# Kernel optimization log

Measured on AMD Instinct MI355X. Metric: run time of the kernel, lower is better.

Reference implementation:

```python
import jax, jax.numpy as jnp
import numpy as np

# static config (mirrors params)
T, B, NA, NF = 48, 256, 23, 4
D = NA * NF          # y_dim = 92
XD = 2               # x_dim
H = 128              # rnn_dim
HD = 128             # h_dim
NL = 2               # n_layers
FS = 0.1
BURN = 12
IN_ENC = XD + D + H  # GRU input size = 222
A0, A1 = 12, 11      # agents 0..11 -> net0, 12..22 -> net1


def setup_inputs() -> dict:
    key = jax.random.key(0)
    ks = jax.random.split(key, 16)
    s = 0.05
    rn = lambda k, shape: jax.random.normal(k, shape, jnp.float32) * s
    return {
        "states": jax.random.normal(ks[0], (T + 1, 1, B, D), jnp.float32),
        # per-network (leading dim 2) GRU layer-0 and layer-1 weights (torch GRU layout: [r|z|n])
        "W_ih0": rn(ks[1], (2, 3 * H, IN_ENC)),
        "W_hh0": rn(ks[2], (2, 3 * H, H)),
        "b_ih0": rn(ks[3], (2, 3 * H)),
        "b_hh0": rn(ks[4], (2, 3 * H)),
        "W_ih1": rn(ks[5], (2, 3 * H, H)),
        "W_hh1": rn(ks[6], (2, 3 * H, H)),
        "b_ih1": rn(ks[7], (2, 3 * H)),
        "b_hh1": rn(ks[8], (2, 3 * H)),
        # decoder MLP (dropout is identity in eval) + mean head
        "W1": rn(ks[9], (2, HD, H)),
        "b1": rn(ks[10], (2, HD)),
        "W2": rn(ks[11], (2, HD, HD)),
        "b2": rn(ks[12], (2, HD)),
        "Wm": rn(ks[13], (2, XD, HD)),
        "bm": rn(ks[14], (2, XD)),
        "rollout": 0,
        "train": 0,
    }


def _gru_cell(x, h, Wih, Whh, bih, bhh):
    gi = x @ Wih.T + bih
    gh = h @ Whh.T + bhh
    r = jax.nn.sigmoid(gi[:, :H] + gh[:, :H])
    z = jax.nn.sigmoid(gi[:, H:2 * H] + gh[:, H:2 * H])
    n = jnp.tanh(gi[:, 2 * H:] + r * gh[:, 2 * H:])
    return (1.0 - z) * n + z * h


def _batch_error(a, b):
    # sum over batch of the euclidean norm over features
    return jnp.sum(jnp.sqrt(jnp.sum((a - b) ** 2, axis=1)))


def _group_step(h, y_t, y3, y3n, lo, hi, g, P):
    # h: [NL, A*B, H]; agents lo..hi-1 of network g, folded into the batch dim
    A = hi - lo
    vel = y3[:, lo:hi, 2:4].transpose(1, 0, 2).reshape(A * B, 2)
    pos = y3[:, lo:hi, 0:2].transpose(1, 0, 2).reshape(A * B, 2)
    vel_true = y3n[:, lo:hi, 2:4].transpose(1, 0, 2).reshape(A * B, 2)
    pos_true = y3n[:, lo:hi, 0:2].transpose(1, 0, 2).reshape(A * B, 2)
    y_rep = jnp.broadcast_to(y_t[None], (A, B, D)).reshape(A * B, D)
    h_last = h[-1]
    enc_in = jnp.concatenate([vel, y_rep, h_last], axis=1)  # [A*B, IN_ENC]
    # decoder uses the PRE-update hidden state
    d = jax.nn.relu(h_last @ P["W1"][g].T + P["b1"][g])
    d = jax.nn.relu(d @ P["W2"][g].T + P["b2"][g])
    dm = d @ P["Wm"][g].T + P["bm"][g]  # [A*B, XD]
    # 2-layer GRU step
    h0n = _gru_cell(enc_in, h[0], P["W_ih0"][g], P["W_hh0"][g], P["b_ih0"][g], P["b_hh0"][g])
    h1n = _gru_cell(h0n, h[1], P["W_ih1"][g], P["W_hh1"][g], P["b_ih1"][g], P["b_hh1"][g])
    h_new = jnp.stack([h0n, h1n])
    L = _batch_error(dm, vel_true)
    ep = _batch_error(pos + vel * FS, pos_true)
    ev = _batch_error(dm[:, :2], vel_true)
    return h_new, L, ep, ev


def _forward(states, P):
    y_seq = states[:T, 0]       # [T, B, D]
    y_next = states[1:T + 1, 0]  # [T, B, D]

    def step(carry, xs):
        h0, h1, L, ep, ev = carry
        y_t, y_t1, t = xs
        y3 = y_t.reshape(B, NA, NF)
        y3n = y_t1.reshape(B, NA, NF)
        h0n, L0, ep0, ev0 = _group_step(h0, y_t, y3, y3n, 0, A0, 0, P)
        h1n, L1, ep1, ev1 = _group_step(h1, y_t, y3, y3n, A0, NA, 1, P)
        m = (t >= BURN).astype(jnp.float32)
        return (h0n, h1n, L + L0 + L1, ep + m * (ep0 + ep1), ev + m * (ev0 + ev1)), None

    init = (jnp.zeros((NL, A0 * B, H), jnp.float32),
            jnp.zeros((NL, A1 * B, H), jnp.float32),
            jnp.zeros((), jnp.float32), jnp.zeros((), jnp.float32), jnp.zeros((), jnp.float32))
    (h0, h1, L, ep, ev), _ = jax.lax.scan(step, init, (y_seq, y_next, jnp.arange(T)))
    L_rec = L / (T * NA)
    e_pos = ep / ((T - BURN) * NA)
    e_vel = ev / ((T - BURN) * NA)
    return L_rec, e_pos, e_vel


def reference(states, W_ih0, W_hh0, b_ih0, b_hh0, W_ih1, W_hh1, b_ih1, b_hh1,
              W1, b1, W2, b2, Wm, bm, rollout, train):
    P = dict(W_ih0=W_ih0, W_hh0=W_hh0, b_ih0=b_ih0, b_hh0=b_hh0,
             W_ih1=W_ih1, W_hh1=W_hh1, b_ih1=b_ih1, b_hh1=b_hh1,
             W1=W1, b1=b1, W2=W2, b2=b2, Wm=Wm, bm=bm)
    return _forward(states, P)
```

## Files before the change

kernel.cpp:

```cpp
#include <hip/hip_runtime.h>
#include <hip/hip_bf16.h>


typedef unsigned short u16;
typedef unsigned int u32;
typedef unsigned char u8;
typedef __attribute__((ext_vector_type(4))) float f32x4;
typedef __attribute__((ext_vector_type(8))) int i32x8;

#define MFMA128(acc, a, b) \
  (acc) = __builtin_amdgcn_mfma_scale_f32_16x16x128_f8f6f4( \
      (a), (b), (acc), 0, 0, 0, 0x7F7F7F7F, 0, 0x7F7F7F7F)

__device__ __forceinline__ i32x8 ld8(const u8* p) { return *(const i32x8*)p; }
__device__ __forceinline__ void pinV(i32x8& x) { asm volatile("" : "+v"(x)); }

__device__ __forceinline__ u8 f2e4(float v) {
  return (u8)(__builtin_amdgcn_cvt_pk_fp8_f32(v, 0.f, 0, false) & 0xff);
}
__device__ __forceinline__ u32 pk4(float a, float b, float c, float d) {
  u32 p = (u32)__builtin_amdgcn_cvt_pk_fp8_f32(a, b, 0, false);
  return (u32)__builtin_amdgcn_cvt_pk_fp8_f32(c, d, (int)p, true);
}
__device__ __forceinline__ float sigf(float x) {
  return __builtin_amdgcn_rcpf(1.f + __expf(-x));
}
__device__ __forceinline__ float tanh_fast(float x) {
  return 1.f - 2.f * __builtin_amdgcn_rcpf(1.f + __expf(2.f * x));
}

constexpr int E0 = 2 * 384 * 352;
constexpr int E1 = E0 + 2 * 384 * 256;
constexpr int E2 = E1 + 2 * 128 * 128;
constexpr int E3 = E2 + 2 * 128 * 128;
constexpr int E4 = E3 + 2 * 128 * 128;
constexpr int E5 = E4 + 2 * 128 * 128;
constexpr int NBIAS = 2048;
constexpr int TOTAL = E5 + NBIAS + 4;
constexpr int WB_BYTE_OFF = 16384;

constexpr int WB0A_REL = E5;
constexpr int YBG2_REL = WB0A_REL + 23 * 384 * 128;
constexpr int NA1 = TOTAL;
constexpr int NA2 = NA1 + 23 * 384 * 128;
constexpr int NA3 = NA2 + 48 * 256 * 128;

__global__ void prep_kernel(const float* __restrict__ states,
                            const float* __restrict__ Wih0, const float* __restrict__ Whh0,
                            const float* __restrict__ bih0, const float* __restrict__ bhh0,
                            const float* __restrict__ Wih1, const float* __restrict__ Whh1,
                            const float* __restrict__ bih1, const float* __restrict__ bhh1,
                            const float* __restrict__ W1, const float* __restrict__ W2,
                            u8* __restrict__ wb, float* __restrict__ wsf) {
  for (int idx = blockIdx.x * blockDim.x + threadIdx.x; idx < NA3;
       idx += gridDim.x * blockDim.x) {
    if (idx < E0) {
      int g = idx / 135168;
      int r = idx - g * 135168;
      int j = r / 352;
      int k = r - j * 352;
      const float* wi = Wih0 + (g * 384 + j) * 222;
      float v;
      if (k < 94) v = wi[k];
      else if (k < 96) v = 0.f;
      else if (k < 224) v = wi[k - 2];
      else v = Whh0[(g * 384 + j) * 128 + (k - 224)];
      wb[idx] = f2e4(v);
    } else if (idx < E1) {
      int q = idx - E0;
      int g = q / 98304;
      int r = q - g * 98304;
      int j = r >> 8;
      int k = r & 255;
      float v = (k < 128) ? Wih1[(g * 384 + j) * 128 + k]
                          : Whh1[(g * 384 + j) * 128 + (k - 128)];
      wb[idx] = f2e4(v);
    } else if (idx < E2) {
      wb[idx] = 0;
    } else if (idx < E3) {
      int q = idx - E2; int g = q >> 14; int r = q & 16383; int j = r >> 7; int k = r & 127;
      wb[idx] = f2e4(W1[(g * 128 + j) * 128 + k]);
    } else if (idx < E4) {
      int q = idx - E3; int g = q >> 14; int r = q & 16383; int j = r >> 7; int k = r & 127;
      wb[idx] = f2e4(W2[(g * 128 + j) * 128 + k]);
    } else if (idx < E5) {
      wb[idx] = 0;
    } else if (idx < E5 + NBIAS) {
      int q = idx - E5;
      float v;
      if (q < 512)       { int g = q >> 8, j = q & 255;              v = bih0[g*384 + j] + bhh0[g*384 + j]; }
      else if (q < 768)  { int p = q - 512;  int g = p >> 7, j = p & 127; v = bih0[g*384 + 256 + j]; }
      else if (q < 1024) { int p = q - 768;  int g = p >> 7, j = p & 127; v = bhh0[g*384 + 256 + j]; }
      else if (q < 1536) { int p = q - 1024; int g = p >> 8, j = p & 255; v = bih1[g*384 + j] + bhh1[g*384 + j]; }
      else if (q < 1792) { int p = q - 1536; int g = p >> 7, j = p & 127; v = bih1[g*384 + 256 + j]; }
      else               { int p = q - 1792; int g = p >> 7, j = p & 127; v = bhh1[g*384 + 256 + j]; }
      wsf[4 + q] = v;
    } else if (idx < TOTAL) {
      wsf[idx - (E5 + NBIAS)] = 0.f;
    } else if (idx < NA2) {
      int q = idx - NA1;
      int a = q / 49152;
      int r = q - a * 49152;
      int j = r >> 7;
      int k = r & 127;
      const float* wi = Wih0 + (((a >= 12) ? 1 : 0) * 384 + j) * 222;
      float v = (k < 92) ? wi[2 + k] : 0.f;
      if (k == a * 4 + 2) v += wi[0];
      if (k == a * 4 + 3) v += wi[1];
      wb[WB0A_REL + q] = f2e4(v);
    } else {
      int q = idx - NA2;
      int t = q >> 15;
      int r = q & 32767;
      int row = r >> 7;
      int k = r & 127;
      float v = (k < 92) ? states[((size_t)t * 256 + row) * 92 + k] : 0.f;
      wb[YBG2_REL + q] = f2e4(v);
    }
  }
}

__global__ __launch_bounds__(512, 2) __attribute__((amdgpu_waves_per_eu(2, 2)))
void rnn_kernel(const float* __restrict__ states,
                const u8* __restrict__ wb,
                float* __restrict__ wsf,
                const float* __restrict__ b1g,
                const float* __restrict__ b2g,
                const float* __restrict__ Wmg,
                const float* __restrict__ bmg) {
  const int blk = blockIdx.x;
  const int g = (blk < 96) ? 0 : 1;
  const int r0 = (g == 0) ? (blk * 32) : ((blk - 96) * 32);
  const int aAg = (g == 0 ? 0 : 12) + (r0 >> 8);
  const int b0 = r0 & 255;

  const int tid = threadIdx.x;
  const int wid = tid >> 6;
  const int ln = tid & 63;
  const int j_in = ln & 15;
  const int kq = ln >> 4;
  const int c0 = wid * 16 + kq * 4;
  const int jh = wid * 16 + j_in;

  __shared__ __align__(16) u8 h0b[2][32 * 144];
  __shared__ __align__(16) u8 h1b[2][32 * 144];
  __shared__ __align__(16) u8 d1b[32 * 144];
  __shared__ __align__(16) u8 d2b[32 * 144];
  __shared__ __align__(16) float bias[1536];
  __shared__ float dmv[48][32][2];
  __shared__ float red[8][3];

  const u8* W0   = wb + g * 135168;
  const u8* W1c  = wb + E0 + g * 98304;
  const u8* Wm1p = wb + E2 + g * 16384;
  const u8* Wm2p = wb + E3 + g * 16384;
  const u8* WB0A = wb + WB0A_REL + aAg * 49152;
  const u8* YBG  = wb + YBG2_REL;

  i32x8 w0r0 = ld8(WB0A + jh * 128 + kq * 32);
  i32x8 w0r1 = ld8(W0 + jh * 352 + 96 + kq * 32);
  i32x8 w0r2 = ld8(W0 + jh * 352 + 224 + kq * 32);
  i32x8 w0z0 = ld8(WB0A + (128 + jh) * 128 + kq * 32);
  i32x8 w0z1 = ld8(W0 + (128 + jh) * 352 + 96 + kq * 32);
  i32x8 w0z2 = ld8(W0 + (128 + jh) * 352 + 224 + kq * 32);
  i32x8 w0n0 = ld8(WB0A + (256 + jh) * 128 + kq * 32);
  i32x8 w0n1 = ld8(W0 + (256 + jh) * 352 + 96 + kq * 32);
  i32x8 wn0  = ld8(W0 + (256 + jh) * 352 + 224 + kq * 32);
  i32x8 w1r0 = ld8(W1c + jh * 256 + kq * 32);
  i32x8 w1r1 = ld8(W1c + jh * 256 + 128 + kq * 32);
  i32x8 w1z0 = ld8(W1c + (128 + jh) * 256 + kq * 32);
  i32x8 w1z1 = ld8(W1c + (128 + jh) * 256 + 128 + kq * 32);
  i32x8 w1n0 = ld8(W1c + (256 + jh) * 256 + kq * 32);
  i32x8 wn1  = ld8(W1c + (256 + jh) * 256 + 128 + kq * 32);
  i32x8 wm1  = ld8(Wm1p + jh * 128 + kq * 32);
  i32x8 wm2  = ld8(Wm2p + jh * 128 + kq * 32);
  pinV(w0r0); pinV(w0r1); pinV(w0r2);
  pinV(w0z0); pinV(w0z1); pinV(w0z2);
  pinV(w0n0); pinV(w0n1); pinV(wn0);
  pinV(w1r0); pinV(w1r1); pinV(w1z0); pinV(w1z1);
  pinV(w1n0); pinV(wn1); pinV(wm1); pinV(wm2);

  for (int i = tid; i < 1536; i += 512) {
    float v;
    if (i < 256)       v = wsf[4 + g * 256 + i];
    else if (i < 384)  v = wsf[516 + g * 128 + (i - 256)];
    else if (i < 512)  v = wsf[772 + g * 128 + (i - 384)];
    else if (i < 768)  v = wsf[1028 + g * 256 + (i - 512)];
    else if (i < 896)  v = wsf[1540 + g * 128 + (i - 768)];
    else if (i < 1024) v = wsf[1796 + g * 128 + (i - 896)];
    else if (i < 1152) v = b1g[g * 128 + (i - 1024)];
    else if (i < 1280) v = b2g[g * 128 + (i - 1152)];
    else               v = Wmg[g * 256 + (i - 1280)];
    bias[i] = v;
  }
  for (int i = tid; i < 32 * 144; i += 512) { h0b[0][i] = 0; h1b[0][i] = 0; }

  f32x4 hv0[2] = {{0,0,0,0},{0,0,0,0}};
  f32x4 hv1[2] = {{0,0,0,0},{0,0,0,0}};
  __syncthreads();

  for (int t = 0; t < 48; ++t) {
    const int cur = t & 1, nxt = cur ^ 1;
    const u8* h0c = h0b[cur]; u8* h0n = h0b[nxt];
    const u8* h1c = h1b[cur]; u8* h1n = h1b[nxt];
    const u8* yt = YBG + t * 32768;

    {
      f32x4 b1v = *(const f32x4*)(bias + 1024 + c0);
      f32x4 brv = *(const f32x4*)(bias + c0);
      f32x4 bzv = *(const f32x4*)(bias + 128 + c0);
      f32x4 biv = *(const f32x4*)(bias + 256 + c0);
      f32x4 bhv = *(const f32x4*)(bias + 384 + c0);
#pragma unroll
      for (int nt = 0; nt < 2; ++nt) {
        const int row = nt * 16 + j_in;
        i32x8 fy  = ld8(yt + (b0 + row) * 128 + kq * 32);
        i32x8 fh1 = ld8(h1c + row * 144 + kq * 32);
        i32x8 fh0 = ld8(h0c + row * 144 + kq * 32);
        f32x4 mm = {0,0,0,0};
        MFMA128(mm, wm1, fh1);
        f32x4 aR = {0,0,0,0}, aZ = {0,0,0,0}, aN = {0,0,0,0}, aG = {0,0,0,0};
        MFMA128(aR, w0r0, fy);  MFMA128(aZ, w0z0, fy);  MFMA128(aN, w0n0, fy);
        MFMA128(aR, w0r1, fh1); MFMA128(aZ, w0z1, fh1); MFMA128(aN, w0n1, fh1);
        MFMA128(aR, w0r2, fh0); MFMA128(aZ, w0z2, fh0); MFMA128(aG, wn0, fh0);
        *(u32*)(d1b + row * 144 + c0) =
          pk4(fmaxf(mm[0]+b1v[0],0.f), fmaxf(mm[1]+b1v[1],0.f),
              fmaxf(mm[2]+b1v[2],0.f), fmaxf(mm[3]+b1v[3],0.f));
#pragma unroll
        for (int i = 0; i < 4; ++i) {
          float rv = sigf(aR[i] + brv[i]);
          float zv = sigf(aZ[i] + bzv[i]);
          float nv = tanh_fast(aN[i] + biv[i] + rv * (aG[i] + bhv[i]));
          hv0[nt][i] = (1.f - zv) * nv + zv * hv0[nt][i];
        }
      }
    }
    __syncthreads();

#pragma unroll
    for (int nt = 0; nt < 2; ++nt)
      *(u32*)(h0n + (nt * 16 + j_in) * 144 + c0) = pk4(hv0[nt][0], hv0[nt][1], hv0[nt][2], hv0[nt][3]);
    {
      f32x4 b2v = *(const f32x4*)(bias + 1152 + c0);
#pragma unroll
      for (int nt = 0; nt < 2; ++nt) {
        const int row = nt * 16 + j_in;
        i32x8 fd1 = ld8(d1b + row * 144 + kq * 32);
        f32x4 mm = {0,0,0,0};
        MFMA128(mm, wm2, fd1);
        *(u32*)(d2b + row * 144 + c0) =
          pk4(fmaxf(mm[0]+b2v[0],0.f), fmaxf(mm[1]+b2v[1],0.f),
              fmaxf(mm[2]+b2v[2],0.f), fmaxf(mm[3]+b2v[3],0.f));
      }
    }
    __syncthreads();

    {
      f32x4 brv = *(const f32x4*)(bias + 512 + c0);
      f32x4 bzv = *(const f32x4*)(bias + 640 + c0);
      f32x4 biv = *(const f32x4*)(bias + 768 + c0);
      f32x4 bhv = *(const f32x4*)(bias + 896 + c0);
#pragma unroll
      for (int nt = 0; nt < 2; ++nt) {
        const int row = nt * 16 + j_in;
        i32x8 fg0 = ld8(h0n + row * 144 + kq * 32);
        i32x8 fh1 = ld8(h1c + row * 144 + kq * 32);
        f32x4 aR = {0,0,0,0}, aZ = {0,0,0,0}, aN = {0,0,0,0}, aG = {0,0,0,0};
        MFMA128(aR, w1r0, fg0); MFMA128(aZ, w1z0, fg0); MFMA128(aN, w1n0, fg0);
        MFMA128(aR, w1r1, fh1); MFMA128(aZ, w1z1, fh1); MFMA128(aG, wn1, fh1);
#pragma unroll
        for (int i = 0; i < 4; ++i) {
          float rv = sigf(aR[i] + brv[i]);
          float zv = sigf(aZ[i] + bzv[i]);
          float nv = tanh_fast(aN[i] + biv[i] + rv * (aG[i] + bhv[i]));
          hv1[nt][i] = (1.f - zv) * nv + zv * hv1[nt][i];
        }
        *(u32*)(h1n + row * 144 + c0) = pk4(hv1[nt][0], hv1[nt][1], hv1[nt][2], hv1[nt][3]);
      }
      {
        int row = tid >> 4, c = (tid >> 3) & 1, part = tid & 7;
        const u8* dp = d2b + row * 144 + part * 16;
        const float* wmr = bias + 1280 + c * 128 + part * 16;
        float s = 0.f;
#pragma unroll
        for (int q = 0; q < 4; ++q) {
          u32 w = *(const u32*)(dp + q * 4);
          s += wmr[q * 4 + 0] * __builtin_amdgcn_cvt_f32_fp8((int)w, 0);
          s += wmr[q * 4 + 1] * __builtin_amdgcn_cvt_f32_fp8((int)w, 1);
          s += wmr[q * 4 + 2] * __builtin_amdgcn_cvt_f32_fp8((int)w, 2);
          s += wmr[q * 4 + 3] * __builtin_amdgcn_cvt_f32_fp8((int)w, 3);
        }
        s += __shfl_xor(s, 1); s += __shfl_xor(s, 2); s += __shfl_xor(s, 4);
        if (part == 0) dmv[t][row][c] = s;
      }
    }
    __syncthreads();
  }

  float accL = 0.f, accEp = 0.f, accEv = 0.f;
  const float bm0 = bmg[g * 2], bm1 = bmg[g * 2 + 1];
  for (int idx = tid; idx < 1536; idx += 512) {
    int t = idx >> 5, row = idx & 31;
    const float* sr = states + ((size_t)(t * 256 + b0 + row)) * 92 + aAg * 4;
    const float* sn = sr + 256 * 92;
    float dx = dmv[t][row][0] + bm0 - sn[2];
    float dy = dmv[t][row][1] + bm1 - sn[3];
    float e = sqrtf(dx * dx + dy * dy);
    accL += e;
    if (t >= 12) {
      accEv += e;
      float ex = sr[0] + 0.1f * sr[2] - sn[0];
      float ey = sr[1] + 0.1f * sr[3] - sn[1];
      accEp += sqrtf(ex * ex + ey * ey);
    }
  }
#pragma unroll
  for (int k = 1; k < 64; k <<= 1) {
    accL  += __shfl_xor(accL, k);
    accEp += __shfl_xor(accEp, k);
    accEv += __shfl_xor(accEv, k);
  }
  if (ln == 0) { red[wid][0] = accL; red[wid][1] = accEp; red[wid][2] = accEv; }
  __syncthreads();
  if (tid < 3) {
    float s = 0.f;
    for (int i = 0; i < 8; ++i) s += red[i][tid];
    atomicAdd(&wsf[tid], s);
  }
}

__global__ void fin_kernel(const float* __restrict__ wacc, float* __restrict__ out) {
  if (threadIdx.x == 0 && blockIdx.x == 0) {
    out[0] = wacc[0] / 1104.f;
    out[1] = wacc[1] / 828.f;
    out[2] = wacc[2] / 828.f;
  }
}

extern "C" void kernel_launch(void* const* d_in, const int* in_sizes, int n_in,
                              void* d_out, int out_size, void* d_ws, size_t ws_size,
                              hipStream_t stream) {
  const float* states = (const float*)d_in[0];
  const float* Wih0 = (const float*)d_in[1];
  const float* Whh0 = (const float*)d_in[2];
  const float* bih0 = (const float*)d_in[3];
  const float* bhh0 = (const float*)d_in[4];
  const float* Wih1 = (const float*)d_in[5];
  const float* Whh1 = (const float*)d_in[6];
  const float* bih1 = (const float*)d_in[7];
  const float* bhh1 = (const float*)d_in[8];
  const float* W1   = (const float*)d_in[9];
  const float* b1   = (const float*)d_in[10];
  const float* W2   = (const float*)d_in[11];
  const float* b2   = (const float*)d_in[12];
  const float* Wm   = (const float*)d_in[13];
  const float* bm   = (const float*)d_in[14];

  float* wsf = (float*)d_ws;
  u8* wb = (u8*)d_ws + WB_BYTE_OFF;

  int prep_blocks = (NA3 + 255) / 256;
  if (prep_blocks > 2048) prep_blocks = 2048;
  prep_kernel<<<prep_blocks, 256, 0, stream>>>(states, Wih0, Whh0, bih0, bhh0,
                                               Wih1, Whh1, bih1, bhh1,
                                               W1, W2, wb, wsf);
  rnn_kernel<<<184, 512, 0, stream>>>(states, wb, wsf, b1, b2, Wm, bm);
  fin_kernel<<<1, 64, 0, stream>>>(wsf, (float*)d_out);
}
```

Before: 287.9 us.

## Cut per-step barriers from three to two and swizzle LDS hidden-state rows

The decoder layer-2 MFMA now runs inside the GRU layer-1 phase, and the mean-head reduction for step t moves into step t+1's first phase, with a tail pass for the last step. This removes one __syncthreads per timestep. LDS rows are padded to 160 bytes with an XOR swizzle of the 32-byte chunks to reduce bank conflicts. The h1 fragments are kept in registers so they are not reloaded, and the packed weight offsets are compacted. The costs are higher register pressure and more complex indexing.

```diff
diff --git a/kernel.cpp b/kernel.cpp
--- a/kernel.cpp
+++ b/kernel.cpp
@@ -27,6 +27,13 @@
 }
 __device__ __forceinline__ float tanh_fast(float x) {
   return 1.f - 2.f * __builtin_amdgcn_rcpf(1.f + __expf(2.f * x));
+}
+
+__device__ __forceinline__ int swz256(int row, int kq) {
+  return row * 160 + ((kq ^ (row & 3)) << 5);
+}
+__device__ __forceinline__ int swzU32(int row, int c0) {
+  return row * 160 + ((((c0 >> 5) ^ (row & 3)) << 5) | (c0 & 31));
 }
 
 constexpr int E0 = 2 * 384 * 352;
@@ -76,12 +83,10 @@
                           : Whh1[(g * 384 + j) * 128 + (k - 128)];
       wb[idx] = f2e4(v);
     } else if (idx < E2) {
-      wb[idx] = 0;
+      int q = idx - E1; int g = q >> 14; int r = q & 16383; int j = r >> 7; int k = r & 127;
+      wb[idx] = f2e4(W1[(g * 128 + j) * 128 + k]);
     } else if (idx < E3) {
       int q = idx - E2; int g = q >> 14; int r = q & 16383; int j = r >> 7; int k = r & 127;
-      wb[idx] = f2e4(W1[(g * 128 + j) * 128 + k]);
-    } else if (idx < E4) {
-      int q = idx - E3; int g = q >> 14; int r = q & 16383; int j = r >> 7; int k = r & 127;
       wb[idx] = f2e4(W2[(g * 128 + j) * 128 + k]);
     } else if (idx < E5) {
       wb[idx] = 0;
@@ -142,18 +147,18 @@
   const int c0 = wid * 16 + kq * 4;
   const int jh = wid * 16 + j_in;
 
-  __shared__ __align__(16) u8 h0b[2][32 * 144];
-  __shared__ __align__(16) u8 h1b[2][32 * 144];
-  __shared__ __align__(16) u8 d1b[32 * 144];
-  __shared__ __align__(16) u8 d2b[32 * 144];
+  __shared__ __align__(16) u8 h0b[2][32 * 160];
+  __shared__ __align__(16) u8 h1b[2][32 * 160];
+  __shared__ __align__(16) u8 d1b[32 * 160];
+  __shared__ __align__(16) u8 d2b[32 * 160];
   __shared__ __align__(16) float bias[1536];
   __shared__ float dmv[48][32][2];
   __shared__ float red[8][3];
 
   const u8* W0   = wb + g * 135168;
   const u8* W1c  = wb + E0 + g * 98304;
-  const u8* Wm1p = wb + E2 + g * 16384;
-  const u8* Wm2p = wb + E3 + g * 16384;
+  const u8* Wm1p = wb + E1 + g * 16384;
+  const u8* Wm2p = wb + E2 + g * 16384;
   const u8* WB0A = wb + WB0A_REL + aAg * 49152;
   const u8* YBG  = wb + YBG2_REL;
 
@@ -193,7 +198,7 @@
     else               v = Wmg[g * 256 + (i - 1280)];
     bias[i] = v;
   }
-  for (int i = tid; i < 32 * 144; i += 512) { h0b[0][i] = 0; h1b[0][i] = 0; }
+  for (int i = tid; i < 32 * 160; i += 512) { h0b[0][i] = 0; h1b[0][i] = 0; }
 
   f32x4 hv0[2] = {{0,0,0,0},{0,0,0,0}};
   f32x4 hv1[2] = {{0,0,0,0},{0,0,0,0}};
@@ -205,6 +210,7 @@
     const u8* h1c = h1b[cur]; u8* h1n = h1b[nxt];
     const u8* yt = YBG + t * 32768;
 
+    i32x8 fh1k[2];
     {
       f32x4 b1v = *(const f32x4*)(bias + 1024 + c0);
       f32x4 brv = *(const f32x4*)(bias + c0);
@@ -215,15 +221,16 @@
       for (int nt = 0; nt < 2; ++nt) {
         const int row = nt * 16 + j_in;
         i32x8 fy  = ld8(yt + (b0 + row) * 128 + kq * 32);
-        i32x8 fh1 = ld8(h1c + row * 144 + kq * 32);
-        i32x8 fh0 = ld8(h0c + row * 144 + kq * 32);
+        i32x8 fh1 = ld8(h1c + swz256(row, kq));
+        i32x8 fh0 = ld8(h0c + swz256(row, kq));
+        fh1k[nt] = fh1;
         f32x4 mm = {0,0,0,0};
         MFMA128(mm, wm1, fh1);
         f32x4 aR = {0,0,0,0}, aZ = {0,0,0,0}, aN = {0,0,0,0}, aG = {0,0,0,0};
         MFMA128(aR, w0r0, fy);  MFMA128(aZ, w0z0, fy);  MFMA128(aN, w0n0, fy);
         MFMA128(aR, w0r1, fh1); MFMA128(aZ, w0z1, fh1); MFMA128(aN, w0n1, fh1);
         MFMA128(aR, w0r2, fh0); MFMA128(aZ, w0z2, fh0); MFMA128(aG, wn0, fh0);
-        *(u32*)(d1b + row * 144 + c0) =
+        *(u32*)(d1b + swzU32(row, c0)) =
           pk4(fmaxf(mm[0]+b1v[0],0.f), fmaxf(mm[1]+b1v[1],0.f),
               fmaxf(mm[2]+b1v[2],0.f), fmaxf(mm[3]+b1v[3],0.f));
 #pragma unroll
@@ -233,29 +240,28 @@
           float nv = tanh_fast(aN[i] + biv[i] + rv * (aG[i] + bhv[i]));
           hv0[nt][i] = (1.f - zv) * nv + zv * hv0[nt][i];
         }
+        *(u32*)(h0n + swzU32(row, c0)) = pk4(hv0[nt][0], hv0[nt][1], hv0[nt][2], hv0[nt][3]);
       }
     }
+    if (t > 0) {
+      int row = tid >> 4, c = (tid >> 3) & 1, part = tid & 7;
+      const float* wmr = bias + 1280 + c * 128 + part * 16;
+      float s = 0.f;
+#pragma unroll
+      for (int q = 0; q < 4; ++q) {
+        u32 w = *(const u32*)(d2b + swzU32(row, part * 16 + q * 4));
+        s += wmr[q * 4 + 0] * __builtin_amdgcn_cvt_f32_fp8((int)w, 0);
+        s += wmr[q * 4 + 1] * __builtin_amdgcn_cvt_f32_fp8((int)w, 1);
+        s += wmr[q * 4 + 2] * __builtin_amdgcn_cvt_f32_fp8((int)w, 2);
+        s += wmr[q * 4 + 3] * __builtin_amdgcn_cvt_f32_fp8((int)w, 3);
+      }
+      s += __shfl_xor(s, 1); s += __shfl_xor(s, 2); s += __shfl_xor(s, 4);
+      if (part == 0) dmv[t - 1][row][c] = s;
+    }
     __syncthreads();
 
-#pragma unroll
-    for (int nt = 0; nt < 2; ++nt)
-      *(u32*)(h0n + (nt * 16 + j_in) * 144 + c0) = pk4(hv0[nt][0], hv0[nt][1], hv0[nt][2], hv0[nt][3]);
     {
       f32x4 b2v = *(const f32x4*)(bias + 1152 + c0);
-#pragma unroll
-      for (int nt = 0; nt < 2; ++nt) {
-        const int row = nt * 16 + j_in;
-        i32x8 fd1 = ld8(d1b + row * 144 + kq * 32);
-        f32x4 mm = {0,0,0,0};
-        MFMA128(mm, wm2, fd1);
-        *(u32*)(d2b + row * 144 + c0) =
-          pk4(fmaxf(mm[0]+b2v[0],0.f), fmaxf(mm[1]+b2v[1],0.f),
-              fmaxf(mm[2]+b2v[2],0.f), fmaxf(mm[3]+b2v[3],0.f));
-      }
-    }
-    __syncthreads();
-
-    {
       f32x4 brv = *(const f32x4*)(bias + 512 + c0);
       f32x4 bzv = *(const f32x4*)(bias + 640 + c0);
       f32x4 biv = *(const f32x4*)(bias + 768 + c0);
@@ -263,11 +269,16 @@
 #pragma unroll
       for (int nt = 0; nt < 2; ++nt) {
         const int row = nt * 16 + j_in;
-        i32x8 fg0 = ld8(h0n + row * 144 + kq * 32);
-        i32x8 fh1 = ld8(h1c + row * 144 + kq * 32);
+        i32x8 fd1 = ld8(d1b + swz256(row, kq));
+        i32x8 fg0 = ld8(h0n + swz256(row, kq));
+        f32x4 mm = {0,0,0,0};
+        MFMA128(mm, wm2, fd1);
         f32x4 aR = {0,0,0,0}, aZ = {0,0,0,0}, aN = {0,0,0,0}, aG = {0,0,0,0};
-        MFMA128(aR, w1r0, fg0); MFMA128(aZ, w1z0, fg0); MFMA128(aN, w1n0, fg0);
-        MFMA128(aR, w1r1, fh1); MFMA128(aZ, w1z1, fh1); MFMA128(aG, wn1, fh1);
+        MFMA128(aR, w1r0, fg0);      MFMA128(aZ, w1z0, fg0);      MFMA128(aN, w1n0, fg0);
+        MFMA128(aR, w1r1, fh1k[nt]); MFMA128(aZ, w1z1, fh1k[nt]); MFMA128(aG, wn1, fh1k[nt]);
+        *(u32*)(d2b + swzU32(row, c0)) =
+          pk4(fmaxf(mm[0]+b2v[0],0.f), fmaxf(mm[1]+b2v[1],0.f),
+              fmaxf(mm[2]+b2v[2],0.f), fmaxf(mm[3]+b2v[3],0.f));
 #pragma unroll
         for (int i = 0; i < 4; ++i) {
           float rv = sigf(aR[i] + brv[i]);
@@ -275,27 +286,28 @@
           float nv = tanh_fast(aN[i] + biv[i] + rv * (aG[i] + bhv[i]));
           hv1[nt][i] = (1.f - zv) * nv + zv * hv1[nt][i];
         }
-        *(u32*)(h1n + row * 144 + c0) = pk4(hv1[nt][0], hv1[nt][1], hv1[nt][2], hv1[nt][3]);
+        *(u32*)(h1n + swzU32(row, c0)) = pk4(hv1[nt][0], hv1[nt][1], hv1[nt][2], hv1[nt][3]);
       }
-      {
-        int row = tid >> 4, c = (tid >> 3) & 1, part = tid & 7;
-        const u8* dp = d2b + row * 144 + part * 16;
-        const float* wmr = bias + 1280 + c * 128 + part * 16;
-        float s = 0.f;
-#pragma unroll
-        for (int q = 0; q < 4; ++q) {
-          u32 w = *(const u32*)(dp + q * 4);
-          s += wmr[q * 4 + 0] * __builtin_amdgcn_cvt_f32_fp8((int)w, 0);
-          s += wmr[q * 4 + 1] * __builtin_amdgcn_cvt_f32_fp8((int)w, 1);
-          s += wmr[q * 4 + 2] * __builtin_amdgcn_cvt_f32_fp8((int)w, 2);
-          s += wmr[q * 4 + 3] * __builtin_amdgcn_cvt_f32_fp8((int)w, 3);
-        }
-        s += __shfl_xor(s, 1); s += __shfl_xor(s, 2); s += __shfl_xor(s, 4);
-        if (part == 0) dmv[t][row][c] = s;
-      }
     }
     __syncthreads();
   }
+
+  {
+    int row = tid >> 4, c = (tid >> 3) & 1, part = tid & 7;
+    const float* wmr = bias + 1280 + c * 128 + part * 16;
+    float s = 0.f;
+#pragma unroll
+    for (int q = 0; q < 4; ++q) {
+      u32 w = *(const u32*)(d2b + swzU32(row, part * 16 + q * 4));
+      s += wmr[q * 4 + 0] * __builtin_amdgcn_cvt_f32_fp8((int)w, 0);
+      s += wmr[q * 4 + 1] * __builtin_amdgcn_cvt_f32_fp8((int)w, 1);
+      s += wmr[q * 4 + 2] * __builtin_amdgcn_cvt_f32_fp8((int)w, 2);
+      s += wmr[q * 4 + 3] * __builtin_amdgcn_cvt_f32_fp8((int)w, 3);
+    }
+    s += __shfl_xor(s, 1); s += __shfl_xor(s, 2); s += __shfl_xor(s, 4);
+    if (part == 0) dmv[47][row][c] = s;
+  }
+  __syncthreads();
 
   float accL = 0.f, accEp = 0.f, accEv = 0.f;
   const float bm0 = bmg[g * 2], bm1 = bmg[g * 2 + 1];
```

Measured after the change: 285.4 us. Within noise of the previous version (-0.8%).
